# Performance work log

Measured on AMD Instinct MI355X. Metric: run time of the kernel, lower is better.

The kernel has to match this reference:

```python
import jax, jax.numpy as jnp
import numpy as np

TOKENS = 8192
HIDDEN = 4096
EPS = 1e-6
FP8_MAX = 448.0  # max finite value of float8_e4m3fn


def setup_inputs() -> dict:
    key = jax.random.key(0)
    k1, k2, k3 = jax.random.split(key, 3)
    x = jax.random.normal(k1, (TOKENS, HIDDEN), jnp.float32)
    # RMSNorm gains near 1
    norm_w = 1.0 + 0.1 * jax.random.normal(k2, (4, HIDDEN), jnp.float32)
    Ws = 0.02 * jax.random.normal(k3, (3, HIDDEN, HIDDEN), jnp.float32)
    # static per-tensor weight scales (amax / fp8_max)
    w_scales = jnp.max(jnp.abs(Ws), axis=(1, 2)) / FP8_MAX
    return {"x": x, "norm_w": norm_w, "Ws": Ws, "w_scales": w_scales}


def _rmsnorm(x, w):
    var = jnp.mean(x * x, axis=-1, keepdims=True)
    return x * jax.lax.rsqrt(var + EPS) * w


def _quant_dequant_fp8(v, s):
    # quantize to e4m3 with scale s, then dequantize (emulated fp8 GEMM inputs)
    q = (v / s).astype(jnp.float8_e4m3fn)
    return q.astype(jnp.float32) * s


def _fp8_linear(y, W, w_scale):
    # dynamic per-token activation scale
    a_scale = jnp.maximum(jnp.max(jnp.abs(y), axis=-1, keepdims=True) / FP8_MAX, 1e-12)
    yq = _quant_dequant_fp8(y, a_scale)           # [T, H]
    Wq = _quant_dequant_fp8(W, w_scale)           # [H, H]
    return yq @ Wq.T                              # torch.nn.Linear convention


def reference(x, norm_w, Ws, w_scales):
    x = jax.nn.relu(x)
    resid = x
    y = _rmsnorm(x, norm_w[0])                    # plain RMSNorm
    for i in range(3):
        h = _fp8_linear(y, Ws[i], w_scales[i])    # FP8 GEMM
        resid = h + resid                         # fused add + RMSNorm
        y = _rmsnorm(resid, norm_w[i + 1])
    return y
```

## Files before the change

### kernel.cpp

```cpp
#include <hip/hip_runtime.h>
#include <stdint.h>

#define TOKENS 8192
#define HIDDEN 4096
constexpr float EPS = 1e-6f;
constexpr float FP8_MAX = 448.0f;

using f32x4  = __attribute__((ext_vector_type(4))) float;
using f32x16 = __attribute__((ext_vector_type(16))) float;
using i32x4  = __attribute__((ext_vector_type(4))) int;
using i32x8  = __attribute__((ext_vector_type(8))) int;

typedef __attribute__((address_space(3))) uint32_t lds_u32_t;
typedef const __attribute__((address_space(1))) uint32_t glb_u32_t;

__device__ inline uint32_t pack_fp8x4(float a, float b, float c, float d) {
    int w = 0;
    w = __builtin_amdgcn_cvt_pk_fp8_f32(a, b, w, false);
    w = __builtin_amdgcn_cvt_pk_fp8_f32(c, d, w, true);
    return (uint32_t)w;
}

__device__ inline float block_sum(float v, float* sh, int tid) {
#pragma unroll
    for (int o = 32; o > 0; o >>= 1) v += __shfl_xor(v, o, 64);
    if ((tid & 63) == 0) sh[tid >> 6] = v;
    __syncthreads();
    return sh[0] + sh[1] + sh[2] + sh[3];
}
__device__ inline float block_max(float v, float* sh, int tid) {
#pragma unroll
    for (int o = 32; o > 0; o >>= 1) v = fmaxf(v, __shfl_xor(v, o, 64));
    if ((tid & 63) == 0) sh[tid >> 6] = v;
    __syncthreads();
    return fmaxf(fmaxf(sh[0], sh[1]), fmaxf(sh[2], sh[3]));
}

__launch_bounds__(256)
__global__ void quant_weights(const float* __restrict__ Ws,
                              const float* __restrict__ w_scales,
                              uint8_t* __restrict__ Wq) {
    size_t idx = ((size_t)blockIdx.x * 256 + threadIdx.x) * 8;
    int tensor = (int)(idx / ((size_t)HIDDEN * HIDDEN));
    float inv = 1.0f / w_scales[tensor];
    const float4* src = (const float4*)(Ws + idx);
    float4 v0 = src[0], v1 = src[1];
    uint2 out;
    out.x = pack_fp8x4(v0.x * inv, v0.y * inv, v0.z * inv, v0.w * inv);
    out.y = pack_fp8x4(v1.x * inv, v1.y * inv, v1.z * inv, v1.w * inv);
    *(uint2*)(Wq + idx) = out;
}

__launch_bounds__(256)
__global__ void relu_rms_quant(const float* __restrict__ x,
                               const float* __restrict__ nw,
                               float* __restrict__ resid,
                               uint8_t* __restrict__ yq,
                               float* __restrict__ ascale) {
    __shared__ float sh1[4], sh2[4];
    const int row = blockIdx.x, tid = threadIdx.x;
    const float* xr = x + (size_t)row * HIDDEN;
    float* rr = resid + (size_t)row * HIDDEN;

    float4 v[4];
    float ss = 0.f;
#pragma unroll
    for (int c = 0; c < 4; ++c) {
        float4 t = *(const float4*)(xr + c * 1024 + tid * 4);
        t.x = fmaxf(t.x, 0.f); t.y = fmaxf(t.y, 0.f);
        t.z = fmaxf(t.z, 0.f); t.w = fmaxf(t.w, 0.f);
        v[c] = t;
        ss += t.x * t.x + t.y * t.y + t.z * t.z + t.w * t.w;
        *(float4*)(rr + c * 1024 + tid * 4) = t;
    }
    ss = block_sum(ss, sh1, tid);
    float rstd = 1.0f / sqrtf(ss * (1.0f / HIDDEN) + EPS);

    float4 y[4];
    float amax = 0.f;
#pragma unroll
    for (int c = 0; c < 4; ++c) {
        float4 w = *(const float4*)(nw + c * 1024 + tid * 4);
        y[c].x = v[c].x * rstd * w.x; amax = fmaxf(amax, fabsf(y[c].x));
        y[c].y = v[c].y * rstd * w.y; amax = fmaxf(amax, fabsf(y[c].y));
        y[c].z = v[c].z * rstd * w.z; amax = fmaxf(amax, fabsf(y[c].z));
        y[c].w = v[c].w * rstd * w.w; amax = fmaxf(amax, fabsf(y[c].w));
    }
    amax = block_max(amax, sh2, tid);
    float s = fmaxf(amax / FP8_MAX, 1e-12f);
    if (tid == 0) ascale[row] = s;
    float inv = 1.0f / s;
#pragma unroll
    for (int c = 0; c < 4; ++c) {
        uint32_t p = pack_fp8x4(y[c].x * inv, y[c].y * inv, y[c].z * inv, y[c].w * inv);
        *(uint32_t*)(yq + (size_t)row * HIDDEN + c * 1024 + tid * 4) = p;
    }
}

__launch_bounds__(256)
__global__ void rms_quant(const float* __restrict__ resid,
                          const float* __restrict__ nw,
                          uint8_t* __restrict__ yq,
                          float* __restrict__ ascale) {
    __shared__ float sh1[4], sh2[4];
    const int row = blockIdx.x, tid = threadIdx.x;
    const float* rr = resid + (size_t)row * HIDDEN;

    float4 v[4];
    float ss = 0.f;
#pragma unroll
    for (int c = 0; c < 4; ++c) {
        float4 t = *(const float4*)(rr + c * 1024 + tid * 4);
        v[c] = t;
        ss += t.x * t.x + t.y * t.y + t.z * t.z + t.w * t.w;
    }
    ss = block_sum(ss, sh1, tid);
    float rstd = 1.0f / sqrtf(ss * (1.0f / HIDDEN) + EPS);

    float4 y[4];
    float amax = 0.f;
#pragma unroll
    for (int c = 0; c < 4; ++c) {
        float4 w = *(const float4*)(nw + c * 1024 + tid * 4);
        y[c].x = v[c].x * rstd * w.x; amax = fmaxf(amax, fabsf(y[c].x));
        y[c].y = v[c].y * rstd * w.y; amax = fmaxf(amax, fabsf(y[c].y));
        y[c].z = v[c].z * rstd * w.z; amax = fmaxf(amax, fabsf(y[c].z));
        y[c].w = v[c].w * rstd * w.w; amax = fmaxf(amax, fabsf(y[c].w));
    }
    amax = block_max(amax, sh2, tid);
    float s = fmaxf(amax / FP8_MAX, 1e-12f);
    if (tid == 0) ascale[row] = s;
    float inv = 1.0f / s;
#pragma unroll
    for (int c = 0; c < 4; ++c) {
        uint32_t p = pack_fp8x4(y[c].x * inv, y[c].y * inv, y[c].z * inv, y[c].w * inv);
        *(uint32_t*)(yq + (size_t)row * HIDDEN + c * 1024 + tid * 4) = p;
    }
}

__launch_bounds__(256)
__global__ void rms_final(const float* __restrict__ resid,
                          const float* __restrict__ nw,
                          float* __restrict__ out) {
    __shared__ float sh1[4];
    const int row = blockIdx.x, tid = threadIdx.x;
    const float* rr = resid + (size_t)row * HIDDEN;

    float4 v[4];
    float ss = 0.f;
#pragma unroll
    for (int c = 0; c < 4; ++c) {
        float4 t = *(const float4*)(rr + c * 1024 + tid * 4);
        v[c] = t;
        ss += t.x * t.x + t.y * t.y + t.z * t.z + t.w * t.w;
    }
    ss = block_sum(ss, sh1, tid);
    float rstd = 1.0f / sqrtf(ss * (1.0f / HIDDEN) + EPS);

#pragma unroll
    for (int c = 0; c < 4; ++c) {
        float4 w = *(const float4*)(nw + c * 1024 + tid * 4);
        float4 o;
        o.x = v[c].x * rstd * w.x;
        o.y = v[c].y * rstd * w.y;
        o.z = v[c].z * rstd * w.z;
        o.w = v[c].w * rstd * w.w;
        *(float4*)(out + (size_t)row * HIDDEN + c * 1024 + tid * 4) = o;
    }
}

#define BM 256
#define BN 256
#define BKB 128

#define MFMA_MX(A, B, C) __builtin_amdgcn_mfma_scale_f32_32x32x64_f8f6f4( \
    (A), (B), (C), 0, 0, 0, 0x7F7F7F7F, 0, 0x7F7F7F7F)

__launch_bounds__(512, 2)
__global__ void gemm_fp8(const uint8_t* __restrict__ Aq,
                         const uint8_t* __restrict__ Bq,
                         const float* __restrict__ ascale,
                         const float* __restrict__ wscale_p,
                         float* __restrict__ resid) {
    __shared__ __align__(16) uint8_t sA[2][BM * BKB];
    __shared__ __align__(16) uint8_t sB[2][BN * BKB];
    __shared__ float s_as[BM];

    const int tid = threadIdx.x;
    int bid = blockIdx.x;
    bid = (bid & 7) * 64 + (bid >> 3);
    const int nbn = HIDDEN / BN;
    const int bm = bid / nbn, bn = bid % nbn;
    const int brow = bm * BM, bcol = bn * BN;

    const int wave = tid >> 6, lane = tid & 63;
    const int wm = wave >> 2, wn = wave & 3;
    const int lr = lane & 31;
    const int lh = lane >> 5;

    if (tid < BM) s_as[tid] = ascale[brow + tid];

    f32x16 acc[4][2] = {};

    const uint8_t* aSrc = Aq + (size_t)brow * HIDDEN;
    const uint8_t* bSrc = Bq + (size_t)bcol * HIDDEN;

    const int r_th = tid >> 3;
    const int gsrc = (tid & 7) ^ (r_th & 7);
    const size_t srcOff = (size_t)r_th * HIDDEN + gsrc * 16;
    const int ldsw = wave * 1024;

    int offA[4][2][2], offB[2][2][2];
#pragma unroll
    for (int mi = 0; mi < 4; ++mi) {
        const int ra = wm * 128 + mi * 32 + lr, s7 = ra & 7;
#pragma unroll
        for (int j = 0; j < 2; ++j)
#pragma unroll
            for (int h2 = 0; h2 < 2; ++h2)
                offA[mi][j][h2] = ra * BKB + ((j * 4 + lh * 2 + h2) ^ s7) * 16;
    }
#pragma unroll
    for (int ni = 0; ni < 2; ++ni) {
        const int rb = wn * 64 + ni * 32 + lr, s7 = rb & 7;
#pragma unroll
        for (int j = 0; j < 2; ++j)
#pragma unroll
            for (int h2 = 0; h2 < 2; ++h2)
                offB[ni][j][h2] = rb * BKB + ((j * 4 + lh * 2 + h2) ^ s7) * 16;
    }

    auto stageHalves = [&](uint8_t* sdst, const uint8_t* src, int kb) {
#pragma unroll
        for (int i = 0; i < 4; ++i) {
            const int rowbase = i * 64;
            __builtin_amdgcn_global_load_lds(
                (glb_u32_t*)(src + (size_t)rowbase * HIDDEN + srcOff + kb),
                (lds_u32_t*)(sdst + rowbase * BKB + ldsw), 16, 0, 0);
        }
    };
    auto rdfrag = [&](const uint8_t* base, const int* off) -> i32x8 {
        i32x4 lo = *(const i32x4*)&base[off[0]];
        i32x4 hi = *(const i32x4*)&base[off[1]];
        return __builtin_shufflevector(lo, hi, 0, 1, 2, 3, 4, 5, 6, 7);
    };

    const int NT = HIDDEN / BKB;
    stageHalves(sA[0], aSrc, 0);
    stageHalves(sB[0], bSrc, 0);
    asm volatile("s_waitcnt vmcnt(0)" ::: "memory");
    __builtin_amdgcn_s_barrier();

#pragma unroll 1
    for (int t = 0; t < NT; ++t) {
        const int buf = t & 1, nbf = buf ^ 1;
        const int kn = (t + 1) * BKB;
        i32x8 a0, a1, a2, a3, b0, b1;

        a0 = rdfrag(sA[buf], offA[0][0]);
        a1 = rdfrag(sA[buf], offA[1][0]);
        b0 = rdfrag(sB[buf], offB[0][0]);
        b1 = rdfrag(sB[buf], offB[1][0]);
        if (t + 1 < NT) stageHalves(sA[nbf], aSrc, kn);
        __builtin_amdgcn_s_barrier();
        asm volatile("s_waitcnt lgkmcnt(0)" ::: "memory");
        __builtin_amdgcn_s_setprio(1);
        acc[0][0] = MFMA_MX(a0, b0, acc[0][0]);
        acc[0][1] = MFMA_MX(a0, b1, acc[0][1]);
        acc[1][0] = MFMA_MX(a1, b0, acc[1][0]);
        acc[1][1] = MFMA_MX(a1, b1, acc[1][1]);
        __builtin_amdgcn_s_setprio(0);
        __builtin_amdgcn_s_barrier();

        a2 = rdfrag(sA[buf], offA[2][0]);
        a3 = rdfrag(sA[buf], offA[3][0]);
        if (t + 1 < NT) stageHalves(sB[nbf], bSrc, kn);
        __builtin_amdgcn_s_barrier();
        asm volatile("s_waitcnt lgkmcnt(0)" ::: "memory");
        __builtin_amdgcn_s_setprio(1);
        acc[2][0] = MFMA_MX(a2, b0, acc[2][0]);
        acc[2][1] = MFMA_MX(a2, b1, acc[2][1]);
        acc[3][0] = MFMA_MX(a3, b0, acc[3][0]);
        acc[3][1] = MFMA_MX(a3, b1, acc[3][1]);
        __builtin_amdgcn_s_setprio(0);
        __builtin_amdgcn_s_barrier();

        a0 = rdfrag(sA[buf], offA[0][1]);
        a1 = rdfrag(sA[buf], offA[1][1]);
        b0 = rdfrag(sB[buf], offB[0][1]);
        b1 = rdfrag(sB[buf], offB[1][1]);
        __builtin_amdgcn_s_barrier();
        asm volatile("s_waitcnt lgkmcnt(0)" ::: "memory");
        __builtin_amdgcn_s_setprio(1);
        acc[0][0] = MFMA_MX(a0, b0, acc[0][0]);
        acc[0][1] = MFMA_MX(a0, b1, acc[0][1]);
        acc[1][0] = MFMA_MX(a1, b0, acc[1][0]);
        acc[1][1] = MFMA_MX(a1, b1, acc[1][1]);
        __builtin_amdgcn_s_setprio(0);
        __builtin_amdgcn_s_barrier();

        a2 = rdfrag(sA[buf], offA[2][1]);
        a3 = rdfrag(sA[buf], offA[3][1]);
        asm volatile("s_waitcnt vmcnt(0)" ::: "memory");
        __builtin_amdgcn_s_barrier();
        asm volatile("s_waitcnt lgkmcnt(0)" ::: "memory");
        __builtin_amdgcn_s_setprio(1);
        acc[2][0] = MFMA_MX(a2, b0, acc[2][0]);
        acc[2][1] = MFMA_MX(a2, b1, acc[2][1]);
        acc[3][0] = MFMA_MX(a3, b0, acc[3][0]);
        acc[3][1] = MFMA_MX(a3, b1, acc[3][1]);
        __builtin_amdgcn_s_setprio(0);
        __builtin_amdgcn_s_barrier();
    }

    const float wsc = *wscale_p;
#pragma unroll
    for (int mi = 0; mi < 4; ++mi) {
        float alpha[16];
#pragma unroll
        for (int i = 0; i < 16; ++i) {
            const int rl = (i & 3) + 8 * (i >> 2) + 4 * lh;
            alpha[i] = s_as[wm * 128 + mi * 32 + rl] * wsc;
        }
#pragma unroll
        for (int ni = 0; ni < 2; ++ni) {
            const int col = bcol + wn * 64 + ni * 32 + lr;
#pragma unroll
            for (int i = 0; i < 16; ++i) {
                const int rl = (i & 3) + 8 * (i >> 2) + 4 * lh;
                const int row_local = wm * 128 + mi * 32 + rl;
                const size_t o = (size_t)(brow + row_local) * HIDDEN + col;
                resid[o] += acc[mi][ni][i] * alpha[i];
            }
        }
    }
}

extern "C" void kernel_launch(void* const* d_in, const int* in_sizes, int n_in,
                              void* d_out, int out_size, void* d_ws, size_t ws_size,
                              hipStream_t stream) {
    const float* x   = (const float*)d_in[0];
    const float* nw  = (const float*)d_in[1];
    const float* Ws  = (const float*)d_in[2];
    const float* wsc = (const float*)d_in[3];
    float* out = (float*)d_out;

    uint8_t* ws = (uint8_t*)d_ws;
    float*   resid  = (float*)ws;
    uint8_t* yq     = ws + (size_t)TOKENS * HIDDEN * 4;
    uint8_t* Wq     = yq + (size_t)TOKENS * HIDDEN;
    float*   ascale = (float*)(Wq + (size_t)3 * HIDDEN * HIDDEN);

    quant_weights<<<(3 * (size_t)HIDDEN * HIDDEN) / 2048, 256, 0, stream>>>(Ws, wsc, Wq);

    relu_rms_quant<<<TOKENS, 256, 0, stream>>>(x, nw, resid, yq, ascale);

    for (int i = 0; i < 3; ++i) {
        gemm_fp8<<<(TOKENS / BM) * (HIDDEN / BN), 512, 0, stream>>>(
            yq, Wq + (size_t)i * HIDDEN * HIDDEN, ascale, wsc + i, resid);
        if (i < 2)
            rms_quant<<<TOKENS, 256, 0, stream>>>(resid, nw + (size_t)(i + 1) * HIDDEN, yq, ascale);
        else
            rms_final<<<TOKENS, 256, 0, stream>>>(resid, nw + (size_t)3 * HIDDEN, out);
    }
}
```

Measured before the change: 698.4 us.

## Restructure FP8 GEMM main loop to one barrier per k-tile with interleaved LDS reads

The main GEMM loop now uses one wait and barrier per k-tile instead of many barriers and lgkmcnt waits per iteration. It issues both A and B next-tile loads up front and interleaves LDS fragment reads with MFMA instructions so the compiler can overlap them. The loop is unrolled by two with fixed buffers. This is meant to cut barrier and synchronisation stalls in the compute-bound inner loop, at the cost of more live registers and relying on the compiler to insert the right LDS waits. It assumes NT is even, which holds because HIDDEN/BKB is a power of two.

```diff
diff --git a/kernel.cpp b/kernel.cpp
--- a/kernel.cpp
+++ b/kernel.cpp
@@ -217,8 +217,8 @@
 #pragma unroll
         for (int j = 0; j < 2; ++j)
 #pragma unroll
-            for (int h2 = 0; h2 < 2; ++h2)
-                offA[mi][j][h2] = ra * BKB + ((j * 4 + lh * 2 + h2) ^ s7) * 16;
+            for (int h = 0; h < 2; ++h)
+                offA[mi][j][h] = ra * BKB + ((j * 4 + lh * 2 + h) ^ s7) * 16;
     }
 #pragma unroll
     for (int ni = 0; ni < 2; ++ni) {
@@ -226,17 +226,20 @@
 #pragma unroll
         for (int j = 0; j < 2; ++j)
 #pragma unroll
-            for (int h2 = 0; h2 < 2; ++h2)
-                offB[ni][j][h2] = rb * BKB + ((j * 4 + lh * 2 + h2) ^ s7) * 16;
-    }
-
-    auto stageHalves = [&](uint8_t* sdst, const uint8_t* src, int kb) {
+            for (int h = 0; h < 2; ++h)
+                offB[ni][j][h] = rb * BKB + ((j * 4 + lh * 2 + h) ^ s7) * 16;
+    }
+
+    auto stage = [&](uint8_t* dstA, uint8_t* dstB, int kb) {
 #pragma unroll
         for (int i = 0; i < 4; ++i) {
             const int rowbase = i * 64;
             __builtin_amdgcn_global_load_lds(
-                (glb_u32_t*)(src + (size_t)rowbase * HIDDEN + srcOff + kb),
-                (lds_u32_t*)(sdst + rowbase * BKB + ldsw), 16, 0, 0);
+                (glb_u32_t*)(aSrc + (size_t)rowbase * HIDDEN + srcOff + kb),
+                (lds_u32_t*)(dstA + rowbase * BKB + ldsw), 16, 0, 0);
+            __builtin_amdgcn_global_load_lds(
+                (glb_u32_t*)(bSrc + (size_t)rowbase * HIDDEN + srcOff + kb),
+                (lds_u32_t*)(dstB + rowbase * BKB + ldsw), 16, 0, 0);
         }
     };
     auto rdfrag = [&](const uint8_t* base, const int* off) -> i32x8 {
@@ -244,73 +247,44 @@
         i32x4 hi = *(const i32x4*)&base[off[1]];
         return __builtin_shufflevector(lo, hi, 0, 1, 2, 3, 4, 5, 6, 7);
     };
+    auto compute = [&](const uint8_t* bA, const uint8_t* bB) {
+        i32x8 b0 = rdfrag(bB, offB[0][0]);
+        i32x8 b1 = rdfrag(bB, offB[1][0]);
+        i32x8 a0 = rdfrag(bA, offA[0][0]);
+        __builtin_amdgcn_s_setprio(1);
+        acc[0][0] = MFMA_MX(a0, b0, acc[0][0]);  i32x8 a1 = rdfrag(bA, offA[1][0]);
+        acc[0][1] = MFMA_MX(a0, b1, acc[0][1]);  i32x8 a2 = rdfrag(bA, offA[2][0]);
+        acc[1][0] = MFMA_MX(a1, b0, acc[1][0]);  i32x8 a3 = rdfrag(bA, offA[3][0]);
+        acc[1][1] = MFMA_MX(a1, b1, acc[1][1]);  i32x8 c0 = rdfrag(bB, offB[0][1]);
+        acc[2][0] = MFMA_MX(a2, b0, acc[2][0]);  i32x8 c1 = rdfrag(bB, offB[1][1]);
+        acc[2][1] = MFMA_MX(a2, b1, acc[2][1]);  i32x8 d0 = rdfrag(bA, offA[0][1]);
+        acc[3][0] = MFMA_MX(a3, b0, acc[3][0]);  i32x8 d1 = rdfrag(bA, offA[1][1]);
+        acc[3][1] = MFMA_MX(a3, b1, acc[3][1]);  i32x8 d2 = rdfrag(bA, offA[2][1]);
+        acc[0][0] = MFMA_MX(d0, c0, acc[0][0]);  i32x8 d3 = rdfrag(bA, offA[3][1]);
+        acc[0][1] = MFMA_MX(d0, c1, acc[0][1]);
+        acc[1][0] = MFMA_MX(d1, c0, acc[1][0]);
+        acc[1][1] = MFMA_MX(d1, c1, acc[1][1]);
+        acc[2][0] = MFMA_MX(d2, c0, acc[2][0]);
+        acc[2][1] = MFMA_MX(d2, c1, acc[2][1]);
+        acc[3][0] = MFMA_MX(d3, c0, acc[3][0]);
+        acc[3][1] = MFMA_MX(d3, c1, acc[3][1]);
+        __builtin_amdgcn_s_setprio(0);
+    };
 
     const int NT = HIDDEN / BKB;
-    stageHalves(sA[0], aSrc, 0);
-    stageHalves(sB[0], bSrc, 0);
-    asm volatile("s_waitcnt vmcnt(0)" ::: "memory");
-    __builtin_amdgcn_s_barrier();
+    stage(sA[0], sB[0], 0);
 
 #pragma unroll 1
-    for (int t = 0; t < NT; ++t) {
-        const int buf = t & 1, nbf = buf ^ 1;
-        const int kn = (t + 1) * BKB;
-        i32x8 a0, a1, a2, a3, b0, b1;
-
-        a0 = rdfrag(sA[buf], offA[0][0]);
-        a1 = rdfrag(sA[buf], offA[1][0]);
-        b0 = rdfrag(sB[buf], offB[0][0]);
-        b1 = rdfrag(sB[buf], offB[1][0]);
-        if (t + 1 < NT) stageHalves(sA[nbf], aSrc, kn);
-        __builtin_amdgcn_s_barrier();
-        asm volatile("s_waitcnt lgkmcnt(0)" ::: "memory");
-        __builtin_amdgcn_s_setprio(1);
-        acc[0][0] = MFMA_MX(a0, b0, acc[0][0]);
-        acc[0][1] = MFMA_MX(a0, b1, acc[0][1]);
-        acc[1][0] = MFMA_MX(a1, b0, acc[1][0]);
-        acc[1][1] = MFMA_MX(a1, b1, acc[1][1]);
-        __builtin_amdgcn_s_setprio(0);
-        __builtin_amdgcn_s_barrier();
-
-        a2 = rdfrag(sA[buf], offA[2][0]);
-        a3 = rdfrag(sA[buf], offA[3][0]);
-        if (t + 1 < NT) stageHalves(sB[nbf], bSrc, kn);
-        __builtin_amdgcn_s_barrier();
-        asm volatile("s_waitcnt lgkmcnt(0)" ::: "memory");
-        __builtin_amdgcn_s_setprio(1);
-        acc[2][0] = MFMA_MX(a2, b0, acc[2][0]);
-        acc[2][1] = MFMA_MX(a2, b1, acc[2][1]);
-        acc[3][0] = MFMA_MX(a3, b0, acc[3][0]);
-        acc[3][1] = MFMA_MX(a3, b1, acc[3][1]);
-        __builtin_amdgcn_s_setprio(0);
-        __builtin_amdgcn_s_barrier();
-
-        a0 = rdfrag(sA[buf], offA[0][1]);
-        a1 = rdfrag(sA[buf], offA[1][1]);
-        b0 = rdfrag(sB[buf], offB[0][1]);
-        b1 = rdfrag(sB[buf], offB[1][1]);
-        __builtin_amdgcn_s_barrier();
-        asm volatile("s_waitcnt lgkmcnt(0)" ::: "memory");
-        __builtin_amdgcn_s_setprio(1);
-        acc[0][0] = MFMA_MX(a0, b0, acc[0][0]);
-        acc[0][1] = MFMA_MX(a0, b1, acc[0][1]);
-        acc[1][0] = MFMA_MX(a1, b0, acc[1][0]);
-        acc[1][1] = MFMA_MX(a1, b1, acc[1][1]);
-        __builtin_amdgcn_s_setprio(0);
-        __builtin_amdgcn_s_barrier();
-
-        a2 = rdfrag(sA[buf], offA[2][1]);
-        a3 = rdfrag(sA[buf], offA[3][1]);
+    for (int t = 0; t < NT; t += 2) {
         asm volatile("s_waitcnt vmcnt(0)" ::: "memory");
         __builtin_amdgcn_s_barrier();
-        asm volatile("s_waitcnt lgkmcnt(0)" ::: "memory");
-        __builtin_amdgcn_s_setprio(1);
-        acc[2][0] = MFMA_MX(a2, b0, acc[2][0]);
-        acc[2][1] = MFMA_MX(a2, b1, acc[2][1]);
-        acc[3][0] = MFMA_MX(a3, b0, acc[3][0]);
-        acc[3][1] = MFMA_MX(a3, b1, acc[3][1]);
-        __builtin_amdgcn_s_setprio(0);
+        stage(sA[1], sB[1], (t + 1) * BKB);
+        compute(sA[0], sB[0]);
+
+        asm volatile("s_waitcnt vmcnt(0)" ::: "memory");
         __builtin_amdgcn_s_barrier();
+        if (t + 2 < NT) stage(sA[0], sB[0], (t + 2) * BKB);
+        compute(sA[1], sB[1]);
     }
 
     const float wsc = *wscale_p;
```

Result: faster. 673.7 us (-3.5%).
